# Optimization experiments

Measured on AMD Instinct MI355X. Metric: run time of the kernel, lower is better.

Reference implementation:

```python
import jax, jax.numpy as jnp
import numpy as np

N = 50000      # nodes
E = 800000     # edges per meta-path
P = 3          # meta-paths
IN = 128       # in_size
OUT = 64       # out_size per head
H = 4          # heads
HID = 128      # semantic-attention hidden
NEG_SLOPE = 0.2


def setup_inputs() -> dict:
    key = jax.random.key(0)
    ks = jax.random.split(key, 8)
    h = jax.random.normal(ks[0], (N, IN), jnp.float32)
    edges = jax.random.randint(ks[1], (P, 2, E), 0, N, dtype=jnp.int32)  # [P, (src,dst), E]
    fc_w = jax.random.normal(ks[2], (P, IN, H * OUT), jnp.float32) * 0.05
    attn_l = jax.random.normal(ks[3], (P, H, OUT), jnp.float32) * 0.05
    attn_r = jax.random.normal(ks[4], (P, H, OUT), jnp.float32) * 0.05
    w1 = jax.random.normal(ks[5], (H * OUT, HID), jnp.float32) * 0.05
    b1 = jnp.zeros((HID,), jnp.float32)
    w2 = jax.random.normal(ks[6], (HID,), jnp.float32) * 0.05
    return {"h": h, "edges": edges, "fc_w": fc_w, "attn_l": attn_l,
            "attn_r": attn_r, "w1": w1, "b1": b1, "w2": w2}


def _gat(h, edge, fc_w, al, ar):
    # One GATConv (DGL semantics, eval mode: dropout off, no residual/bias).
    src, dst = edge[0], edge[1]
    feat = (h @ fc_w).reshape(N, H, OUT)                 # [N,H,D]
    el = jnp.einsum('nhd,hd->nh', feat, al)              # [N,H]
    er = jnp.einsum('nhd,hd->nh', feat, ar)
    e = jax.nn.leaky_relu(el[src] + er[dst], NEG_SLOPE)  # [E,H]
    # edge softmax over incoming edges of each dst node
    m = jax.ops.segment_max(e, dst, num_segments=N)      # [N,H]
    m = jnp.where(jnp.isfinite(m), m, 0.0)               # empty segments -> 0
    ex = jnp.exp(e - m[dst])
    s = jax.ops.segment_sum(ex, dst, num_segments=N)     # [N,H]
    alpha = ex / s[dst]                                  # [E,H]
    msg = feat[src] * alpha[:, :, None]                  # [E,H,D]
    rst = jax.ops.segment_sum(msg, dst, num_segments=N)  # [N,H,D]
    return jax.nn.elu(rst).reshape(N, H * OUT)


def reference(h, edges, fc_w, attn_l, attn_r, w1, b1, w2):
    # per-meta-path GAT embeddings -> [N, P, H*OUT]
    z = jnp.stack([_gat(h, edges[i], fc_w[i], attn_l[i], attn_r[i])
                   for i in range(P)], axis=1)
    # semantic attention: Linear -> tanh -> Linear(no bias) -> softmax over P
    w = jnp.tanh(z @ w1 + b1) @ w2                       # [N,P]
    beta = jax.nn.softmax(w, axis=1)[:, :, None]         # [N,P,1]
    return (beta * z).sum(axis=1)                        # [N, H*OUT]
```

## Files before the change

kernel.cpp:

```cpp
#include <hip/hip_runtime.h>
#include <hip/hip_bf16.h>
#include <hip/hip_fp16.h>

#define N_NODES 50000
#define N_EDGES 800000
#define N_PATHS 3
#define IN_F    128
#define HO      256
#define N_HEADS 4
#define HID     128

#define BLK_PER_PATH 32
#define EDGES_PER_HB 25000
#define HIST_BLOCKS  (N_PATHS * BLK_PER_PATH)
#define NPACK        12500
#define FEAT_RB      782
#define SCAT_PP      782
#define GATH_PP      12500
#define FEAT_ELEMS   ((size_t)N_NODES * HO)

typedef __bf16 bf16;
typedef __bf16 bf16x8 __attribute__((ext_vector_type(8)));
typedef float  f32x4  __attribute__((ext_vector_type(4)));
typedef unsigned short u16;
typedef unsigned char  u8;
typedef unsigned int   u32;

__global__ __launch_bounds__(256) void k_prep(const float* __restrict__ fc_w,
                                              const float* __restrict__ w1,
                                              bf16* __restrict__ fcwT,
                                              bf16* __restrict__ w1T) {
    int g = blockIdx.x * 256 + threadIdx.x;
    if (g < N_PATHS * IN_F * HO) {
        int p = g >> 15, r = g & 32767;
        int col = r & 255, k = r >> 8;
        fcwT[(size_t)p * 32768 + col * IN_F + k] = (bf16)fc_w[(size_t)p * 32768 + k * HO + col];
    } else {
        int gg = g - N_PATHS * IN_F * HO;
        if (gg < HO * HID) {
            int k = gg & 255, j = gg >> 8;
            w1T[(size_t)j * HO + k] = (bf16)w1[(size_t)k * HID + j];
        }
    }
}

__device__ __forceinline__ void hist_role(int b, const int* __restrict__ edges,
                                          u32* __restrict__ cnt32, u8* __restrict__ lrank,
                                          u32* hist) {
    const int p = b / BLK_PER_PATH, blk = b - p * BLK_PER_PATH;
    const int t = threadIdx.x;
    for (int i = t; i < NPACK; i += 256) hist[i] = 0;
    __syncthreads();

    const int* dstp = edges + (size_t)p * 2 * N_EDGES + N_EDGES + blk * EDGES_PER_HB;
    u8* lr = lrank + (size_t)p * N_EDGES + blk * EDGES_PER_HB;
    for (int q = t; q < EDGES_PER_HB / 4; q += 256) {
        int4 d4 = ((const int4*)dstp)[q];
        u32 o0 = atomicAdd(&hist[d4.x >> 2], 1u << ((d4.x & 3) * 8));
        u32 o1 = atomicAdd(&hist[d4.y >> 2], 1u << ((d4.y & 3) * 8));
        u32 o2 = atomicAdd(&hist[d4.z >> 2], 1u << ((d4.z & 3) * 8));
        u32 o3 = atomicAdd(&hist[d4.w >> 2], 1u << ((d4.w & 3) * 8));
        uchar4 r4;
        r4.x = (u8)(o0 >> ((d4.x & 3) * 8));
        r4.y = (u8)(o1 >> ((d4.y & 3) * 8));
        r4.z = (u8)(o2 >> ((d4.z & 3) * 8));
        r4.w = (u8)(o3 >> ((d4.w & 3) * 8));
        ((uchar4*)lr)[q] = r4;
    }
    __syncthreads();
    u32* out = cnt32 + (size_t)b * NPACK;
    for (int i = t; i < NPACK; i += 256) out[i] = hist[i];
}

__device__ __forceinline__ void feat_role(int rb, const float* __restrict__ h,
                                          const bf16* __restrict__ fcwT,
                                          const float* __restrict__ al,
                                          const float* __restrict__ ar,
                                          __half* __restrict__ featAll,
                                          float* __restrict__ elAll,
                                          float* __restrict__ erAll) {
    const int t = threadIdx.x, w = t >> 6, l = t & 63, lo = l & 15, hi = l >> 4;
    const int arow = rb * 64 + w * 16 + lo;
    const int crow = rb * 64 + w * 16 + hi * 4;

    bf16x8 afr[4];
    if (arow < N_NODES) {
        const float* hp = h + (size_t)arow * IN_F;
#pragma unroll
        for (int ks = 0; ks < 4; ++ks) {
            float4 f0 = *(const float4*)(hp + ks * 32 + hi * 8);
            float4 f1 = *(const float4*)(hp + ks * 32 + hi * 8 + 4);
            bf16x8 a;
            a[0]=(bf16)f0.x; a[1]=(bf16)f0.y; a[2]=(bf16)f0.z; a[3]=(bf16)f0.w;
            a[4]=(bf16)f1.x; a[5]=(bf16)f1.y; a[6]=(bf16)f1.z; a[7]=(bf16)f1.w;
            afr[ks] = a;
        }
    } else {
#pragma unroll
        for (int ks = 0; ks < 4; ++ks) { bf16x8 a = {}; afr[ks] = a; }
    }

    for (int p = 0; p < N_PATHS; ++p) {
        __half* feat = featAll + (size_t)p * FEAT_ELEMS;
        const float* alp = al + p * HO;
        const float* arp = ar + p * HO;
        float* elA = elAll + (size_t)p * N_NODES * 4;
        float* erA = erAll + (size_t)p * N_NODES * 4;
#pragma unroll
        for (int ch = 0; ch < 2; ++ch) {
            const bf16* W = fcwT + (size_t)p * 32768 + (size_t)ch * 128 * IN_F;
            f32x4 acc[8];
#pragma unroll
            for (int c = 0; c < 8; ++c) { f32x4 zz = {0.f,0.f,0.f,0.f}; acc[c] = zz; }
#pragma unroll
            for (int ctl = 0; ctl < 8; ++ctl) {
                const bf16* wp = W + (size_t)(ctl * 16 + lo) * IN_F + hi * 8;
                f32x4 a = acc[ctl];
#pragma unroll
                for (int ks = 0; ks < 4; ++ks)
                    a = __builtin_amdgcn_mfma_f32_16x16x32_bf16(afr[ks], *(const bf16x8*)(wp + ks * 32), a, 0, 0, 0);
                acc[ctl] = a;
            }
            float elP[2][4] = {{0}}, erP[2][4] = {{0}};
#pragma unroll
            for (int ctl = 0; ctl < 8; ++ctl) {
                const int gcol = ch * 128 + ctl * 16 + lo;
                const float av = alp[gcol], bv = arp[gcol];
                const int hl = ctl >> 2;
#pragma unroll
                for (int rr = 0; rr < 4; ++rr) {
                    float v = acc[ctl][rr];
                    elP[hl][rr] = fmaf(v, av, elP[hl][rr]);
                    erP[hl][rr] = fmaf(v, bv, erP[hl][rr]);
                    if (crow + rr < N_NODES)
                        feat[(size_t)(crow + rr) * HO + gcol] = __float2half(v);
                }
            }
#pragma unroll
            for (int hl = 0; hl < 2; ++hl)
#pragma unroll
                for (int rr = 0; rr < 4; ++rr) {
                    float v = elP[hl][rr], u = erP[hl][rr];
#pragma unroll
                    for (int m = 1; m <= 8; m <<= 1) {
                        v += __shfl_xor(v, m, 64);
                        u += __shfl_xor(u, m, 64);
                    }
                    elP[hl][rr] = v; erP[hl][rr] = u;
                }
            if (lo == 0) {
#pragma unroll
                for (int rr = 0; rr < 4; ++rr) {
                    if (crow + rr < N_NODES) {
                        *(float2*)&elA[(crow + rr) * 4 + ch * 2] = make_float2(elP[0][rr], elP[1][rr]);
                        *(float2*)&erA[(crow + rr) * 4 + ch * 2] = make_float2(erP[0][rr], erP[1][rr]);
                    }
                }
            }
        }
    }
}

__global__ __launch_bounds__(256) void k_hf(const int* __restrict__ edges,
                                            u32* __restrict__ cnt32,
                                            u8* __restrict__ lrank,
                                            const float* __restrict__ h,
                                            const bf16* __restrict__ fcwT,
                                            const float* __restrict__ al,
                                            const float* __restrict__ ar,
                                            __half* __restrict__ featAll,
                                            float* __restrict__ elAll,
                                            float* __restrict__ erAll) {
    __shared__ u32 hist[NPACK];
    const int bid = blockIdx.x;
    if (bid < HIST_BLOCKS)
        hist_role(bid, edges, cnt32, lrank, hist);
    else
        feat_role(bid - HIST_BLOCKS, h, fcwT, al, ar, featAll, elAll, erAll);
}

__global__ __launch_bounds__(256) void k_base(u32* __restrict__ cnt32,
                                              int* __restrict__ deg) {
    int g = blockIdx.x * 256 + threadIdx.x;
    if (g >= N_PATHS * NPACK) return;
    int p = g / NPACK, q = g - p * NPACK;
    u32 s0 = 0, s1 = 0, s2 = 0, s3 = 0;
#pragma unroll
    for (int blk = 0; blk < BLK_PER_PATH; ++blk) {
        size_t idx = (size_t)(p * BLK_PER_PATH + blk) * NPACK + q;
        u32 c = cnt32[idx];
        cnt32[idx] = s0 | (s1 << 8) | (s2 << 16) | (s3 << 24);
        s0 += c & 0xff; s1 += (c >> 8) & 0xff; s2 += (c >> 16) & 0xff; s3 += c >> 24;
    }
    int4 d4 = {(int)s0, (int)s1, (int)s2, (int)s3};
    *(int4*)(deg + (size_t)p * N_NODES + 4 * q) = d4;
}

__global__ __launch_bounds__(1024) void k_scan(const int* __restrict__ deg,
                                               int* __restrict__ rowptr) {
    __shared__ int part[1024];
    const int p = blockIdx.x;
    const int* dg = deg + p * N_NODES;
    int* rp = rowptr + p * (N_NODES + 1);

    const int tid = threadIdx.x;
    const int CH = (N_NODES + 1023) / 1024;
    const int start = tid * CH;
    int s = 0;
    for (int i = 0; i < CH; ++i) { int idx = start + i; if (idx < N_NODES) s += dg[idx]; }
    part[tid] = s;
    __syncthreads();
    for (int off = 1; off < 1024; off <<= 1) {
        int v = (tid >= off) ? part[tid - off] : 0;
        __syncthreads();
        part[tid] += v;
        __syncthreads();
    }
    int excl = (tid == 0) ? 0 : part[tid - 1];
    for (int i = 0; i < CH; ++i) {
        int idx = start + i;
        if (idx < N_NODES) { rp[idx] = excl; excl += dg[idx]; }
    }
    if (tid == 1023) rp[N_NODES] = N_EDGES;
}

__device__ __forceinline__ void scatter_role(int b, int p, const int* __restrict__ edges,
                                             const u8* __restrict__ lrank,
                                             const u32* __restrict__ cnt32,
                                             const int* __restrict__ rowptr,
                                             u16* __restrict__ csrAll) {
    int e = (b * 256 + threadIdx.x) * 4;
    if (e >= N_EDGES) return;
    const int blk = e / EDGES_PER_HB;
    const int* ep = edges + (size_t)p * 2 * N_EDGES;
    int4 s4 = *(const int4*)(ep + e);
    int4 d4 = *(const int4*)(ep + N_EDGES + e);
    uchar4 r4 = *(const uchar4*)(lrank + (size_t)p * N_EDGES + e);
    const int* rp = rowptr + p * (N_NODES + 1);
    const u32* bb = cnt32 + (size_t)(p * BLK_PER_PATH + blk) * NPACK;
    u16* c = csrAll + (size_t)p * N_EDGES;
    int p0 = rp[d4.x] + (int)((bb[d4.x >> 2] >> ((d4.x & 3) * 8)) & 0xff) + r4.x;
    int p1 = rp[d4.y] + (int)((bb[d4.y >> 2] >> ((d4.y & 3) * 8)) & 0xff) + r4.y;
    int p2 = rp[d4.z] + (int)((bb[d4.z >> 2] >> ((d4.z & 3) * 8)) & 0xff) + r4.z;
    int p3 = rp[d4.w] + (int)((bb[d4.w >> 2] >> ((d4.w & 3) * 8)) & 0xff) + r4.w;
    c[p0] = (u16)s4.x; c[p1] = (u16)s4.y; c[p2] = (u16)s4.z; c[p3] = (u16)s4.w;
}

__device__ __forceinline__ void gather_role(int nb, int p,
                                            const u16* __restrict__ csrAll,
                                            const int* __restrict__ rowptrAll,
                                            const float4* __restrict__ elAll,
                                            const float4* __restrict__ erAll,
                                            const __half* __restrict__ featAll,
                                            bf16* __restrict__ z,
                                            u32 (*s_off)[64], __half2 (*s_ad)[4][66]) {
    const int t = threadIdx.x, w = t >> 6, l = t & 63;
    const int half = l >> 5, c = l & 31, hh = c >> 3;
    const int n = nb * 4 + w;

    const u16*    csr    = csrAll + (size_t)p * N_EDGES;
    const int*    rowptr = rowptrAll + p * (N_NODES + 1);
    const float4* el4    = elAll + (size_t)p * N_NODES;
    const __half* feat   = featAll + (size_t)p * FEAT_ELEMS;

    const int b0 = rowptr[n], b1e = rowptr[n + 1];
    const float4 er_n = (erAll + (size_t)p * N_NODES)[n];

    __half2 acc0 = __float2half2_rn(0.f), acc1 = acc0, acc2 = acc0, acc3 = acc0;
    float4 den = {0.f, 0.f, 0.f, 0.f};

    for (int base = b0; base < b1e; base += 64) {
        const int cnt = min(64, b1e - base);
        if (l < cnt) {
            int sv = csr[base + l];
            s_off[w][l] = (u32)(sv * HO);
            float4 e = el4[sv];
            float vx = e.x + er_n.x, vy = e.y + er_n.y,
                  vz = e.z + er_n.z, vw = e.w + er_n.w;
            vx = (vx >= 0.f) ? vx : 0.2f * vx;
            vy = (vy >= 0.f) ? vy : 0.2f * vy;
            vz = (vz >= 0.f) ? vz : 0.2f * vz;
            vw = (vw >= 0.f) ? vw : 0.2f * vw;
            float ex = __expf(vx), ey = __expf(vy), ez = __expf(vz), ew = __expf(vw);
            den.x += ex; den.y += ey; den.z += ez; den.w += ew;
            s_ad[w][0][l] = __float2half2_rn(ex);
            s_ad[w][1][l] = __float2half2_rn(ey);
            s_ad[w][2][l] = __float2half2_rn(ez);
            s_ad[w][3][l] = __float2half2_rn(ew);
        }
        int i2 = 0;
        for (; i2 + 4 <= cnt; i2 += 4) {
            const int e1 = i2 + half, e2 = i2 + 2 + half;
            u32 o1 = s_off[w][e1], o2 = s_off[w][e2];
            __half2 a1 = s_ad[w][hh][e1], a2v = s_ad[w][hh][e2];
            const uint4 u1 = *(const uint4*)(feat + o1 + c * 8);
            const uint4 u2 = *(const uint4*)(feat + o2 + c * 8);
            acc0 = __hfma2(__builtin_bit_cast(__half2, u1.x), a1, acc0);
            acc1 = __hfma2(__builtin_bit_cast(__half2, u1.y), a1, acc1);
            acc2 = __hfma2(__builtin_bit_cast(__half2, u1.z), a1, acc2);
            acc3 = __hfma2(__builtin_bit_cast(__half2, u1.w), a1, acc3);
            acc0 = __hfma2(__builtin_bit_cast(__half2, u2.x), a2v, acc0);
            acc1 = __hfma2(__builtin_bit_cast(__half2, u2.y), a2v, acc1);
            acc2 = __hfma2(__builtin_bit_cast(__half2, u2.z), a2v, acc2);
            acc3 = __hfma2(__builtin_bit_cast(__half2, u2.w), a2v, acc3);
        }
        for (; i2 < cnt; i2 += 2) {
            const int e = i2 + half;
            if (e < cnt) {
                u32 o1 = s_off[w][e];
                __half2 a1 = s_ad[w][hh][e];
                const uint4 u = *(const uint4*)(feat + o1 + c * 8);
                acc0 = __hfma2(__builtin_bit_cast(__half2, u.x), a1, acc0);
                acc1 = __hfma2(__builtin_bit_cast(__half2, u.y), a1, acc1);
                acc2 = __hfma2(__builtin_bit_cast(__half2, u.z), a1, acc2);
                acc3 = __hfma2(__builtin_bit_cast(__half2, u.w), a1, acc3);
            }
        }
    }

    float s[8];
    { float2 f0 = __half22float2(acc0), f1 = __half22float2(acc1),
             f2 = __half22float2(acc2), f3 = __half22float2(acc3);
      s[0]=f0.x; s[1]=f0.y; s[2]=f1.x; s[3]=f1.y; s[4]=f2.x; s[5]=f2.y; s[6]=f3.x; s[7]=f3.y; }
#pragma unroll
    for (int j = 0; j < 8; ++j) s[j] += __shfl_xor(s[j], 32, 64);
#pragma unroll
    for (int off = 32; off; off >>= 1) {
        den.x += __shfl_xor(den.x, off, 64);
        den.y += __shfl_xor(den.y, off, 64);
        den.z += __shfl_xor(den.z, off, 64);
        den.w += __shfl_xor(den.w, off, 64);
    }
    const float d = (hh == 0) ? den.x : (hh == 1) ? den.y : (hh == 2) ? den.z : den.w;
    const float inv = (d > 0.f) ? 1.f / d : 0.f;
    if (half == 0) {
        bf16x8 ov;
#pragma unroll
        for (int j = 0; j < 8; ++j) {
            float v = s[j] * inv;
            v = (v > 0.f) ? v : expm1f(v);
            ov[j] = (bf16)v;
        }
        *(bf16x8*)(z + (size_t)n * (N_PATHS * HO) + p * HO + c * 8) = ov;
    }
}

__global__ __launch_bounds__(256) void k_gs(int gp, int sp,
                                            const int* __restrict__ edges,
                                            const u8* __restrict__ lrank,
                                            const u32* __restrict__ cnt32,
                                            const int* __restrict__ rowptr,
                                            u16* __restrict__ csr,
                                            const float4* __restrict__ el,
                                            const float4* __restrict__ er,
                                            const __half* __restrict__ feat,
                                            bf16* __restrict__ z) {
    __shared__ u32     s_off[4][64];
    __shared__ __half2 s_ad[4][4][66];
    const int bid = blockIdx.x;
    if (bid < SCAT_PP) {
        if (sp >= 0) scatter_role(bid, sp, edges, lrank, cnt32, rowptr, csr);
    } else if (gp >= 0) {
        gather_role(bid - SCAT_PP, gp, csr, rowptr, el, er, feat, z, s_off, s_ad);
    }
}

__global__ __launch_bounds__(256) void k_semout(const bf16* __restrict__ z,
                                                const bf16* __restrict__ w1T,
                                                const float* __restrict__ b1,
                                                const float* __restrict__ w2,
                                                float* __restrict__ out) {
    __shared__ bf16  zs[48 * 264];
    __shared__ float psem[4][48];
    __shared__ float betas[16][4];

    const int t = threadIdx.x, w = t >> 6, l = t & 63;
    const int lo = l & 15, hi = l >> 4;
    const int n0 = blockIdx.x * 16;

    bf16x8 bfr[2][8];
#pragma unroll
    for (int ct = 0; ct < 2; ++ct) {
        const int j = (2 * w + ct) * 16 + lo;
#pragma unroll
        for (int s = 0; s < 8; ++s)
            bfr[ct][s] = *(const bf16x8*)(w1T + (size_t)j * HO + s * 32 + hi * 8);
    }

    const uint4* zg4 = (const uint4*)(z + (size_t)n0 * (N_PATHS * HO));
    for (int i = t; i < 1536; i += 256) {
        uint4 v = zg4[i];
        int r = i >> 5, cin = (i & 31) * 8;
        *(uint4*)&zs[r * 264 + cin] = v;
    }
    __syncthreads();

    f32x4 acc[2][3];
#pragma unroll
    for (int ct = 0; ct < 2; ++ct)
#pragma unroll
        for (int m = 0; m < 3; ++m) { f32x4 zz = {0.f,0.f,0.f,0.f}; acc[ct][m] = zz; }

    for (int s = 0; s < 8; ++s) {
#pragma unroll
        for (int m = 0; m < 3; ++m) {
            bf16x8 a = *(const bf16x8*)&zs[(m * 16 + lo) * 264 + s * 32 + hi * 8];
            acc[0][m] = __builtin_amdgcn_mfma_f32_16x16x32_bf16(a, bfr[0][s], acc[0][m], 0, 0, 0);
            acc[1][m] = __builtin_amdgcn_mfma_f32_16x16x32_bf16(a, bfr[1][s], acc[1][m], 0, 0, 0);
        }
    }

    const int j0 = (2 * w + 0) * 16 + lo;
    const int j1 = (2 * w + 1) * 16 + lo;
    const float b1_0 = b1[j0], w2_0 = w2[j0];
    const float b1_1 = b1[j1], w2_1 = w2[j1];
#pragma unroll
    for (int m = 0; m < 3; ++m) {
#pragma unroll
        for (int r = 0; r < 4; ++r) {
            float tt = tanhf(acc[0][m][r] + b1_0) * w2_0
                     + tanhf(acc[1][m][r] + b1_1) * w2_1;
            tt += __shfl_xor(tt, 1, 64);
            tt += __shfl_xor(tt, 2, 64);
            tt += __shfl_xor(tt, 4, 64);
            tt += __shfl_xor(tt, 8, 64);
            if (lo == 0) psem[w][m * 16 + hi * 4 + r] = tt;
        }
    }
    __syncthreads();
    if (t < 48) psem[0][t] = psem[0][t] + psem[1][t] + psem[2][t] + psem[3][t];
    __syncthreads();
    if (t < 16) {
        float a0 = psem[0][3 * t], a1 = psem[0][3 * t + 1], a2 = psem[0][3 * t + 2];
        float mx = fmaxf(a0, fmaxf(a1, a2));
        float e0 = __expf(a0 - mx), e1 = __expf(a1 - mx), e2 = __expf(a2 - mx);
        float is = 1.f / (e0 + e1 + e2);
        betas[t][0] = e0 * is; betas[t][1] = e1 * is; betas[t][2] = e2 * is;
    }
    __syncthreads();
    for (int i = 0; i < 16; ++i) {
        float bb0 = betas[i][0], bb1 = betas[i][1], bb2 = betas[i][2];
        float o = bb0 * (float)zs[(3 * i + 0) * 264 + t]
                + bb1 * (float)zs[(3 * i + 1) * 264 + t]
                + bb2 * (float)zs[(3 * i + 2) * 264 + t];
        out[(size_t)(n0 + i) * HO + t] = o;
    }
}

static inline size_t align256(size_t x) { return (x + 255) & ~(size_t)255; }

extern "C" void kernel_launch(void* const* d_in, const int* in_sizes, int n_in,
                              void* d_out, int out_size, void* d_ws, size_t ws_size,
                              hipStream_t stream) {
    const float* h     = (const float*)d_in[0];
    const int*   edges = (const int*)d_in[1];
    const float* fc_w  = (const float*)d_in[2];
    const float* al    = (const float*)d_in[3];
    const float* ar    = (const float*)d_in[4];
    const float* w1    = (const float*)d_in[5];
    const float* b1    = (const float*)d_in[6];
    const float* w2    = (const float*)d_in[7];
    float* out = (float*)d_out;

    char* base = (char*)d_ws;
    size_t off = 0;
    auto carve = [&](size_t bytes) -> char* {
        char* p = base + off; off = align256(off + bytes); return p;
    };
    __half* feat   = (__half*)carve((size_t)N_PATHS * FEAT_ELEMS * 2);
    bf16*   zbuf   = (bf16*)carve((size_t)N_NODES * N_PATHS * HO * 2);
    u16*    csr    = (u16*)carve((size_t)N_PATHS * N_EDGES * 2);
    bf16*   fcwT   = (bf16*)carve((size_t)N_PATHS * IN_F * HO * 2);
    bf16*   w1T    = (bf16*)carve((size_t)HO * HID * 2);
    float*  el     = (float*)carve((size_t)N_PATHS * N_NODES * 4 * 4);
    float*  er     = (float*)carve((size_t)N_PATHS * N_NODES * 4 * 4);
    int*    deg    = (int*)carve((size_t)N_PATHS * N_NODES * 4);
    int*    rowptr = (int*)carve((size_t)N_PATHS * (N_NODES + 1) * 4);
    u8*     lrank  = (u8*)carve((size_t)N_PATHS * N_EDGES);
    u32*    cnt32  = (u32*)carve((size_t)HIST_BLOCKS * NPACK * 4);
    (void)ws_size; (void)in_sizes; (void)n_in; (void)out_size;

    k_prep<<<512, 256, 0, stream>>>(fc_w, w1, fcwT, w1T);
    k_hf<<<HIST_BLOCKS + FEAT_RB, 256, 0, stream>>>(
        edges, cnt32, lrank, h, fcwT, al, ar, feat, el, er);
    k_base<<<(N_PATHS * NPACK + 255) / 256, 256, 0, stream>>>(cnt32, deg);
    k_scan<<<N_PATHS, 1024, 0, stream>>>(deg, rowptr);
    k_gs<<<SCAT_PP, 256, 0, stream>>>(-1, 0, edges, lrank, cnt32, rowptr, csr,
                                      (const float4*)el, (const float4*)er, feat, zbuf);
    k_gs<<<SCAT_PP + GATH_PP, 256, 0, stream>>>(0, 1, edges, lrank, cnt32, rowptr, csr,
                                      (const float4*)el, (const float4*)er, feat, zbuf);
    k_gs<<<SCAT_PP + GATH_PP, 256, 0, stream>>>(1, 2, edges, lrank, cnt32, rowptr, csr,
                                      (const float4*)el, (const float4*)er, feat, zbuf);
    k_gs<<<SCAT_PP + GATH_PP, 256, 0, stream>>>(2, -1, edges, lrank, cnt32, rowptr, csr,
                                      (const float4*)el, (const float4*)er, feat, zbuf);
    k_semout<<<N_NODES / 16, 256, 0, stream>>>(zbuf, w1T, b1, w2, out);
}
```

Measured before the change: 486.9 us.

## Regroup kernel stages: fuse prep+hist, scatter+feat, and gather all paths at once

Reorganizes the pipeline. Weight prep is now co-launched with the histogram, using more and smaller histogram blocks. The scatter for all three paths runs alongside the feature GEMM in one launch, and a single gather kernel covers all three meta-paths instead of three interleaved scatter/gather launches. The gather inner loop is also unrolled to issue four feature loads per iteration for more memory-level parallelism. This cuts launch count and serialization, at the cost of more histogram partial buffers for k_base to scan and higher register pressure in the gather.

```diff
diff --git a/kernel.cpp b/kernel.cpp
--- a/kernel.cpp
+++ b/kernel.cpp
@@ -10,13 +10,13 @@
 #define N_HEADS 4
 #define HID     128
 
-#define BLK_PER_PATH 32
-#define EDGES_PER_HB 25000
+#define BLK_PER_PATH 80
+#define EDGES_PER_HB 10000
 #define HIST_BLOCKS  (N_PATHS * BLK_PER_PATH)
+#define PREP_BLOCKS  512
 #define NPACK        12500
 #define FEAT_RB      782
-#define SCAT_PP      782
-#define GATH_PP      12500
+#define SCAT_BLOCKS  2344
 #define FEAT_ELEMS   ((size_t)N_NODES * HO)
 
 typedef __bf16 bf16;
@@ -26,11 +26,11 @@
 typedef unsigned char  u8;
 typedef unsigned int   u32;
 
-__global__ __launch_bounds__(256) void k_prep(const float* __restrict__ fc_w,
-                                              const float* __restrict__ w1,
-                                              bf16* __restrict__ fcwT,
-                                              bf16* __restrict__ w1T) {
-    int g = blockIdx.x * 256 + threadIdx.x;
+__device__ __forceinline__ void prep_role(int b, const float* __restrict__ fc_w,
+                                          const float* __restrict__ w1,
+                                          bf16* __restrict__ fcwT,
+                                          bf16* __restrict__ w1T) {
+    int g = b * 256 + threadIdx.x;
     if (g < N_PATHS * IN_F * HO) {
         int p = g >> 15, r = g & 32767;
         int col = r & 255, k = r >> 8;
@@ -72,6 +72,90 @@
     for (int i = t; i < NPACK; i += 256) out[i] = hist[i];
 }
 
+__global__ __launch_bounds__(256) void k_ph(const float* __restrict__ fc_w,
+                                            const float* __restrict__ w1,
+                                            bf16* __restrict__ fcwT,
+                                            bf16* __restrict__ w1T,
+                                            const int* __restrict__ edges,
+                                            u32* __restrict__ cnt32,
+                                            u8* __restrict__ lrank) {
+    __shared__ u32 hist[NPACK];
+    const int bid = blockIdx.x;
+    if (bid < PREP_BLOCKS)
+        prep_role(bid, fc_w, w1, fcwT, w1T);
+    else
+        hist_role(bid - PREP_BLOCKS, edges, cnt32, lrank, hist);
+}
+
+__global__ __launch_bounds__(256) void k_base(u32* __restrict__ cnt32,
+                                              int* __restrict__ deg) {
+    int g = blockIdx.x * 256 + threadIdx.x;
+    if (g >= N_PATHS * NPACK) return;
+    int p = g / NPACK, q = g - p * NPACK;
+    u32 s0 = 0, s1 = 0, s2 = 0, s3 = 0;
+#pragma unroll 8
+    for (int blk = 0; blk < BLK_PER_PATH; ++blk) {
+        size_t idx = (size_t)(p * BLK_PER_PATH + blk) * NPACK + q;
+        u32 c = cnt32[idx];
+        cnt32[idx] = s0 | (s1 << 8) | (s2 << 16) | (s3 << 24);
+        s0 += c & 0xff; s1 += (c >> 8) & 0xff; s2 += (c >> 16) & 0xff; s3 += c >> 24;
+    }
+    int4 d4 = {(int)s0, (int)s1, (int)s2, (int)s3};
+    *(int4*)(deg + (size_t)p * N_NODES + 4 * q) = d4;
+}
+
+__global__ __launch_bounds__(1024) void k_scan(const int* __restrict__ deg,
+                                               int* __restrict__ rowptr) {
+    __shared__ int part[1024];
+    const int p = blockIdx.x;
+    const int* dg = deg + p * N_NODES;
+    int* rp = rowptr + p * (N_NODES + 1);
+
+    const int tid = threadIdx.x;
+    const int CH = (N_NODES + 1023) / 1024;
+    const int start = tid * CH;
+    int s = 0;
+    for (int i = 0; i < CH; ++i) { int idx = start + i; if (idx < N_NODES) s += dg[idx]; }
+    part[tid] = s;
+    __syncthreads();
+    for (int off = 1; off < 1024; off <<= 1) {
+        int v = (tid >= off) ? part[tid - off] : 0;
+        __syncthreads();
+        part[tid] += v;
+        __syncthreads();
+    }
+    int excl = (tid == 0) ? 0 : part[tid - 1];
+    for (int i = 0; i < CH; ++i) {
+        int idx = start + i;
+        if (idx < N_NODES) { rp[idx] = excl; excl += dg[idx]; }
+    }
+    if (tid == 1023) rp[N_NODES] = N_EDGES;
+}
+
+__device__ __forceinline__ void scatter_role(int b, const int* __restrict__ edges,
+                                             const u8* __restrict__ lrank,
+                                             const u32* __restrict__ cnt32,
+                                             const int* __restrict__ rowptr,
+                                             u16* __restrict__ csrAll) {
+    int gt = b * 256 + threadIdx.x;
+    if (gt >= (N_PATHS * N_EDGES) / 4) return;
+    int base = gt * 4;
+    int p = base / N_EDGES, e = base - p * N_EDGES;
+    const int blk = e / EDGES_PER_HB;
+    const int* ep = edges + (size_t)p * 2 * N_EDGES;
+    int4 s4 = *(const int4*)(ep + e);
+    int4 d4 = *(const int4*)(ep + N_EDGES + e);
+    uchar4 r4 = *(const uchar4*)(lrank + base);
+    const int* rp = rowptr + p * (N_NODES + 1);
+    const u32* bb = cnt32 + (size_t)(p * BLK_PER_PATH + blk) * NPACK;
+    u16* c = csrAll + (size_t)p * N_EDGES;
+    int p0 = rp[d4.x] + (int)((bb[d4.x >> 2] >> ((d4.x & 3) * 8)) & 0xff) + r4.x;
+    int p1 = rp[d4.y] + (int)((bb[d4.y >> 2] >> ((d4.y & 3) * 8)) & 0xff) + r4.y;
+    int p2 = rp[d4.z] + (int)((bb[d4.z >> 2] >> ((d4.z & 3) * 8)) & 0xff) + r4.z;
+    int p3 = rp[d4.w] + (int)((bb[d4.w >> 2] >> ((d4.w & 3) * 8)) & 0xff) + r4.w;
+    c[p0] = (u16)s4.x; c[p1] = (u16)s4.y; c[p2] = (u16)s4.z; c[p3] = (u16)s4.w;
+}
+
 __device__ __forceinline__ void feat_role(int rb, const float* __restrict__ h,
                                           const bf16* __restrict__ fcwT,
                                           const float* __restrict__ al,
@@ -161,9 +245,11 @@
     }
 }
 
-__global__ __launch_bounds__(256) void k_hf(const int* __restrict__ edges,
-                                            u32* __restrict__ cnt32,
-                                            u8* __restrict__ lrank,
+__global__ __launch_bounds__(256) void k_sf(const int* __restrict__ edges,
+                                            const u8* __restrict__ lrank,
+                                            const u32* __restrict__ cnt32,
+                                            const int* __restrict__ rowptr,
+                                            u16* __restrict__ csr,
                                             const float* __restrict__ h,
                                             const bf16* __restrict__ fcwT,
                                             const float* __restrict__ al,
@@ -171,89 +257,25 @@
                                             __half* __restrict__ featAll,
                                             float* __restrict__ elAll,
                                             float* __restrict__ erAll) {
-    __shared__ u32 hist[NPACK];
     const int bid = blockIdx.x;
-    if (bid < HIST_BLOCKS)
-        hist_role(bid, edges, cnt32, lrank, hist);
+    if (bid < SCAT_BLOCKS)
+        scatter_role(bid, edges, lrank, cnt32, rowptr, csr);
     else
-        feat_role(bid - HIST_BLOCKS, h, fcwT, al, ar, featAll, elAll, erAll);
-}
-
-__global__ __launch_bounds__(256) void k_base(u32* __restrict__ cnt32,
-                                              int* __restrict__ deg) {
-    int g = blockIdx.x * 256 + threadIdx.x;
-    if (g >= N_PATHS * NPACK) return;
-    int p = g / NPACK, q = g - p * NPACK;
-    u32 s0 = 0, s1 = 0, s2 = 0, s3 = 0;
-#pragma unroll
-    for (int blk = 0; blk < BLK_PER_PATH; ++blk) {
-        size_t idx = (size_t)(p * BLK_PER_PATH + blk) * NPACK + q;
-        u32 c = cnt32[idx];
-        cnt32[idx] = s0 | (s1 << 8) | (s2 << 16) | (s3 << 24);
-        s0 += c & 0xff; s1 += (c >> 8) & 0xff; s2 += (c >> 16) & 0xff; s3 += c >> 24;
-    }
-    int4 d4 = {(int)s0, (int)s1, (int)s2, (int)s3};
-    *(int4*)(deg + (size_t)p * N_NODES + 4 * q) = d4;
-}
-
-__global__ __launch_bounds__(1024) void k_scan(const int* __restrict__ deg,
-                                               int* __restrict__ rowptr) {
-    __shared__ int part[1024];
-    const int p = blockIdx.x;
-    const int* dg = deg + p * N_NODES;
-    int* rp = rowptr + p * (N_NODES + 1);
-
-    const int tid = threadIdx.x;
-    const int CH = (N_NODES + 1023) / 1024;
-    const int start = tid * CH;
-    int s = 0;
-    for (int i = 0; i < CH; ++i) { int idx = start + i; if (idx < N_NODES) s += dg[idx]; }
-    part[tid] = s;
-    __syncthreads();
-    for (int off = 1; off < 1024; off <<= 1) {
-        int v = (tid >= off) ? part[tid - off] : 0;
-        __syncthreads();
-        part[tid] += v;
-        __syncthreads();
-    }
-    int excl = (tid == 0) ? 0 : part[tid - 1];
-    for (int i = 0; i < CH; ++i) {
-        int idx = start + i;
-        if (idx < N_NODES) { rp[idx] = excl; excl += dg[idx]; }
-    }
-    if (tid == 1023) rp[N_NODES] = N_EDGES;
-}
-
-__device__ __forceinline__ void scatter_role(int b, int p, const int* __restrict__ edges,
-                                             const u8* __restrict__ lrank,
-                                             const u32* __restrict__ cnt32,
-                                             const int* __restrict__ rowptr,
-                                             u16* __restrict__ csrAll) {
-    int e = (b * 256 + threadIdx.x) * 4;
-    if (e >= N_EDGES) return;
-    const int blk = e / EDGES_PER_HB;
-    const int* ep = edges + (size_t)p * 2 * N_EDGES;
-    int4 s4 = *(const int4*)(ep + e);
-    int4 d4 = *(const int4*)(ep + N_EDGES + e);
-    uchar4 r4 = *(const uchar4*)(lrank + (size_t)p * N_EDGES + e);
-    const int* rp = rowptr + p * (N_NODES + 1);
-    const u32* bb = cnt32 + (size_t)(p * BLK_PER_PATH + blk) * NPACK;
-    u16* c = csrAll + (size_t)p * N_EDGES;
-    int p0 = rp[d4.x] + (int)((bb[d4.x >> 2] >> ((d4.x & 3) * 8)) & 0xff) + r4.x;
-    int p1 = rp[d4.y] + (int)((bb[d4.y >> 2] >> ((d4.y & 3) * 8)) & 0xff) + r4.y;
-    int p2 = rp[d4.z] + (int)((bb[d4.z >> 2] >> ((d4.z & 3) * 8)) & 0xff) + r4.z;
-    int p3 = rp[d4.w] + (int)((bb[d4.w >> 2] >> ((d4.w & 3) * 8)) & 0xff) + r4.w;
-    c[p0] = (u16)s4.x; c[p1] = (u16)s4.y; c[p2] = (u16)s4.z; c[p3] = (u16)s4.w;
-}
-
-__device__ __forceinline__ void gather_role(int nb, int p,
-                                            const u16* __restrict__ csrAll,
-                                            const int* __restrict__ rowptrAll,
-                                            const float4* __restrict__ elAll,
-                                            const float4* __restrict__ erAll,
-                                            const __half* __restrict__ featAll,
-                                            bf16* __restrict__ z,
-                                            u32 (*s_off)[64], __half2 (*s_ad)[4][66]) {
+        feat_role(bid - SCAT_BLOCKS, h, fcwT, al, ar, featAll, elAll, erAll);
+}
+
+__global__ __launch_bounds__(256) void k_gather3(const u16* __restrict__ csrAll,
+                                                 const int* __restrict__ rowptrAll,
+                                                 const float4* __restrict__ elAll,
+                                                 const float4* __restrict__ erAll,
+                                                 const __half* __restrict__ featAll,
+                                                 bf16* __restrict__ z) {
+    __shared__ u32     s_off[4][64];
+    __shared__ __half2 s_ad[4][4][66];
+    const int pb = blockIdx.x;
+    const int p  = pb / (N_NODES / 4);
+    const int nb = pb - p * (N_NODES / 4);
+
     const int t = threadIdx.x, w = t >> 6, l = t & 63;
     const int half = l >> 5, c = l & 31, hh = c >> 3;
     const int n = nb * 4 + w;
@@ -289,31 +311,58 @@
             s_ad[w][3][l] = __float2half2_rn(ew);
         }
         int i2 = 0;
-        for (; i2 + 4 <= cnt; i2 += 4) {
-            const int e1 = i2 + half, e2 = i2 + 2 + half;
-            u32 o1 = s_off[w][e1], o2 = s_off[w][e2];
-            __half2 a1 = s_ad[w][hh][e1], a2v = s_ad[w][hh][e2];
+        for (; i2 + 8 <= cnt; i2 += 8) {
+            const int e0 = i2 + half, e1 = i2 + 2 + half,
+                      e2 = i2 + 4 + half, e3 = i2 + 6 + half;
+            u32 o0 = s_off[w][e0], o1 = s_off[w][e1], o2 = s_off[w][e2], o3 = s_off[w][e3];
+            __half2 a0 = s_ad[w][hh][e0], a1 = s_ad[w][hh][e1],
+                    a2 = s_ad[w][hh][e2], a3 = s_ad[w][hh][e3];
+            const uint4 u0 = *(const uint4*)(feat + o0 + c * 8);
             const uint4 u1 = *(const uint4*)(feat + o1 + c * 8);
             const uint4 u2 = *(const uint4*)(feat + o2 + c * 8);
+            const uint4 u3 = *(const uint4*)(feat + o3 + c * 8);
+            acc0 = __hfma2(__builtin_bit_cast(__half2, u0.x), a0, acc0);
+            acc1 = __hfma2(__builtin_bit_cast(__half2, u0.y), a0, acc1);
+            acc2 = __hfma2(__builtin_bit_cast(__half2, u0.z), a0, acc2);
+            acc3 = __hfma2(__builtin_bit_cast(__half2, u0.w), a0, acc3);
             acc0 = __hfma2(__builtin_bit_cast(__half2, u1.x), a1, acc0);
             acc1 = __hfma2(__builtin_bit_cast(__half2, u1.y), a1, acc1);
             acc2 = __hfma2(__builtin_bit_cast(__half2, u1.z), a1, acc2);
             acc3 = __hfma2(__builtin_bit_cast(__half2, u1.w), a1, acc3);
-            acc0 = __hfma2(__builtin_bit_cast(__half2, u2.x), a2v, acc0);
-            acc1 = __hfma2(__builtin_bit_cast(__half2, u2.y), a2v, acc1);
-            acc2 = __hfma2(__builtin_bit_cast(__half2, u2.z), a2v, acc2);
-            acc3 = __hfma2(__builtin_bit_cast(__half2, u2.w), a2v, acc3);
+            acc0 = __hfma2(__builtin_bit_cast(__half2, u2.x), a2, acc0);
+            acc1 = __hfma2(__builtin_bit_cast(__half2, u2.y), a2, acc1);
+            acc2 = __hfma2(__builtin_bit_cast(__half2, u2.z), a2, acc2);
+            acc3 = __hfma2(__builtin_bit_cast(__half2, u2.w), a2, acc3);
+            acc0 = __hfma2(__builtin_bit_cast(__half2, u3.x), a3, acc0);
+            acc1 = __hfma2(__builtin_bit_cast(__half2, u3.y), a3, acc1);
+            acc2 = __hfma2(__builtin_bit_cast(__half2, u3.z), a3, acc2);
+            acc3 = __hfma2(__builtin_bit_cast(__half2, u3.w), a3, acc3);
+        }
+        for (; i2 + 4 <= cnt; i2 += 4) {
+            const int e0 = i2 + half, e1 = i2 + 2 + half;
+            u32 o0 = s_off[w][e0], o1 = s_off[w][e1];
+            __half2 a0 = s_ad[w][hh][e0], a1 = s_ad[w][hh][e1];
+            const uint4 u0 = *(const uint4*)(feat + o0 + c * 8);
+            const uint4 u1 = *(const uint4*)(feat + o1 + c * 8);
+            acc0 = __hfma2(__builtin_bit_cast(__half2, u0.x), a0, acc0);
+            acc1 = __hfma2(__builtin_bit_cast(__half2, u0.y), a0, acc1);
+            acc2 = __hfma2(__builtin_bit_cast(__half2, u0.z), a0, acc2);
+            acc3 = __hfma2(__builtin_bit_cast(__half2, u0.w), a0, acc3);
+            acc0 = __hfma2(__builtin_bit_cast(__half2, u1.x), a1, acc0);
+            acc1 = __hfma2(__builtin_bit_cast(__half2, u1.y), a1, acc1);
+            acc2 = __hfma2(__builtin_bit_cast(__half2, u1.z), a1, acc2);
+            acc3 = __hfma2(__builtin_bit_cast(__half2, u1.w), a1, acc3);
         }
         for (; i2 < cnt; i2 += 2) {
             const int e = i2 + half;
             if (e < cnt) {
-                u32 o1 = s_off[w][e];
-                __half2 a1 = s_ad[w][hh][e];
-                const uint4 u = *(const uint4*)(feat + o1 + c * 8);
-                acc0 = __hfma2(__builtin_bit_cast(__half2, u.x), a1, acc0);
-                acc1 = __hfma2(__builtin_bit_cast(__half2, u.y), a1, acc1);
-                acc2 = __hfma2(__builtin_bit_cast(__half2, u.z), a1, acc2);
-                acc3 = __hfma2(__builtin_bit_cast(__half2, u.w), a1, acc3);
+                u32 o0 = s_off[w][e];
+                __half2 a0 = s_ad[w][hh][e];
+                const uint4 u = *(const uint4*)(feat + o0 + c * 8);
+                acc0 = __hfma2(__builtin_bit_cast(__half2, u.x), a0, acc0);
+                acc1 = __hfma2(__builtin_bit_cast(__half2, u.y), a0, acc1);
+                acc2 = __hfma2(__builtin_bit_cast(__half2, u.z), a0, acc2);
+                acc3 = __hfma2(__builtin_bit_cast(__half2, u.w), a0, acc3);
             }
         }
     }
@@ -342,26 +391,6 @@
             ov[j] = (bf16)v;
         }
         *(bf16x8*)(z + (size_t)n * (N_PATHS * HO) + p * HO + c * 8) = ov;
-    }
-}
-
-__global__ __launch_bounds__(256) void k_gs(int gp, int sp,
-                                            const int* __restrict__ edges,
-                                            const u8* __restrict__ lrank,
-                                            const u32* __restrict__ cnt32,
-                                            const int* __restrict__ rowptr,
-                                            u16* __restrict__ csr,
-                                            const float4* __restrict__ el,
-                                            const float4* __restrict__ er,
-                                            const __half* __restrict__ feat,
-                                            bf16* __restrict__ z) {
-    __shared__ u32     s_off[4][64];
-    __shared__ __half2 s_ad[4][4][66];
-    const int bid = blockIdx.x;
-    if (bid < SCAT_PP) {
-        if (sp >= 0) scatter_role(bid, sp, edges, lrank, cnt32, rowptr, csr);
-    } else if (gp >= 0) {
-        gather_role(bid - SCAT_PP, gp, csr, rowptr, el, er, feat, z, s_off, s_ad);
     }
 }
 
@@ -480,18 +509,13 @@
     u32*    cnt32  = (u32*)carve((size_t)HIST_BLOCKS * NPACK * 4);
     (void)ws_size; (void)in_sizes; (void)n_in; (void)out_size;
 
-    k_prep<<<512, 256, 0, stream>>>(fc_w, w1, fcwT, w1T);
-    k_hf<<<HIST_BLOCKS + FEAT_RB, 256, 0, stream>>>(
-        edges, cnt32, lrank, h, fcwT, al, ar, feat, el, er);
+    k_ph<<<PREP_BLOCKS + HIST_BLOCKS, 256, 0, stream>>>(
+        fc_w, w1, fcwT, w1T, edges, cnt32, lrank);
     k_base<<<(N_PATHS * NPACK + 255) / 256, 256, 0, stream>>>(cnt32, deg);
     k_scan<<<N_PATHS, 1024, 0, stream>>>(deg, rowptr);
-    k_gs<<<SCAT_PP, 256, 0, stream>>>(-1, 0, edges, lrank, cnt32, rowptr, csr,
-                                      (const float4*)el, (const float4*)er, feat, zbuf);
-    k_gs<<<SCAT_PP + GATH_PP, 256, 0, stream>>>(0, 1, edges, lrank, cnt32, rowptr, csr,
-                                      (const float4*)el, (const float4*)er, feat, zbuf);
-    k_gs<<<SCAT_PP + GATH_PP, 256, 0, stream>>>(1, 2, edges, lrank, cnt32, rowptr, csr,
-                                      (const float4*)el, (const float4*)er, feat, zbuf);
-    k_gs<<<SCAT_PP + GATH_PP, 256, 0, stream>>>(2, -1, edges, lrank, cnt32, rowptr, csr,
-                                      (const float4*)el, (const float4*)er, feat, zbuf);
+    k_sf<<<SCAT_BLOCKS + FEAT_RB, 256, 0, stream>>>(
+        edges, lrank, cnt32, rowptr, csr, h, fcwT, al, ar, feat, el, er);
+    k_gather3<<<N_PATHS * (N_NODES / 4), 256, 0, stream>>>(
+        csr, rowptr, (const float4*)el, (const float4*)er, feat, zbuf);
     k_semout<<<N_NODES / 16, 256, 0, stream>>>(zbuf, w1T, b1, w2, out);
 }
```

Result: no change. 487.6 us, median of 2 (+0.1%).
